# Performance work log

Measured on AMD Instinct MI355X. Metric: run time of the kernel, lower is better.

## Reference

```python
import jax, jax.numpy as jnp
import numpy as np

N, E, G = 25000, 400000, 64
IN, HID, OUT = 16, 16, 16
EF, EH, NH, NC = 8, 64, 128, 10
EPS = 1e-5


def _seg_mean(vals, idx, n):
    s = jax.ops.segment_sum(vals, idx, num_segments=n)
    c = jax.ops.segment_sum(jnp.ones((idx.shape[0], 1), vals.dtype), idx, num_segments=n)
    return s / jnp.maximum(c, 1.0)


def _bn(x, g, b):
    m = x.mean(axis=0)
    v = x.var(axis=0)
    return (x - m) * jax.lax.rsqrt(v + EPS) * g + b


def _nnconv(x, src, dst, ew, root, bias, n_nodes, out_ch):
    # ew: [E, in*out] -> per-edge weight matrix [E, in, out]
    ew = ew.reshape(ew.shape[0], x.shape[1], out_ch)
    msg = jnp.einsum('ei,eio->eo', x[src], ew)  # gather + per-edge matmul
    agg = _seg_mean(msg, dst, n_nodes)          # scatter-mean at target nodes
    return x @ root + agg + bias


def setup_inputs():
    key = jax.random.key(0)
    ks = jax.random.split(key, 24)
    f = lambda k, shp, sc: jax.random.normal(k, shp, dtype=jnp.float32) * sc
    inp = {
        'x': f(ks[0], (N, IN), 1.0),
        'edge_src': jax.random.randint(ks[1], (E,), 0, N, dtype=jnp.int32),
        'edge_dst': jax.random.randint(ks[2], (E,), 0, N, dtype=jnp.int32),
        'edge_attr': f(ks[3], (E, EF), 1.0),
        'batch': jnp.sort(jax.random.randint(ks[4], (N,), 0, G, dtype=jnp.int32)),
        # edge MLP 1: Linear(EF,EH) -> ReLU -> Linear(EH, IN*HID)
        'en1_w1': f(ks[5], (EF, EH), 0.3), 'en1_b1': jnp.zeros((EH,), jnp.float32),
        'en1_w2': f(ks[6], (EH, IN * HID), 0.1), 'en1_b2': jnp.zeros((IN * HID,), jnp.float32),
        'root1': f(ks[7], (IN, HID), 0.25), 'bias1': jnp.zeros((HID,), jnp.float32),
        'bn1_g': jnp.ones((HID,), jnp.float32), 'bn1_b': jnp.zeros((HID,), jnp.float32),
        # edge net 2 (FC): single Linear(EF, HID*OUT)
        'en2_w': f(ks[8], (EF, HID * OUT), 0.1), 'en2_b': jnp.zeros((HID * OUT,), jnp.float32),
        'root2': f(ks[9], (HID, OUT), 0.25), 'bias2': jnp.zeros((OUT,), jnp.float32),
        'bn2_g': jnp.ones((OUT,), jnp.float32), 'bn2_b': jnp.zeros((OUT,), jnp.float32),
        'mlp_w1': f(ks[10], (OUT, NH), 0.25), 'mlp_b1': jnp.zeros((NH,), jnp.float32),
        'mlp_w2': f(ks[11], (NH, NC), 0.1), 'mlp_b2': jnp.zeros((NC,), jnp.float32),
    }
    return inp


def reference(x, edge_src, edge_dst, edge_attr, batch,
              en1_w1, en1_b1, en1_w2, en1_b2, root1, bias1, bn1_g, bn1_b,
              en2_w, en2_b, root2, bias2, bn2_g, bn2_b,
              mlp_w1, mlp_b1, mlp_w2, mlp_b2):
    # NNConv layer 1 (edge MLP -> per-edge weight -> gather-matmul-scatter-mean)
    ew1 = jax.nn.relu(edge_attr @ en1_w1 + en1_b1) @ en1_w2 + en1_b2
    h = _nnconv(x, edge_src, edge_dst, ew1, root1, bias1, N, HID)
    h = _bn(h, bn1_g, bn1_b)
    # NNConv layer 2 (single-Linear edge net)
    ew2 = edge_attr @ en2_w + en2_b
    h = _nnconv(h, edge_src, edge_dst, ew2, root2, bias2, N, OUT)
    h = _bn(h, bn2_g, bn2_b)
    # graph-level mean pooling
    g = _seg_mean(h, batch, G)
    # MLP head + log_softmax
    logits = jax.nn.relu(g @ mlp_w1 + mlp_b1) @ mlp_w2 + mlp_b2
    return jax.nn.log_softmax(logits, axis=1)
```

## Files before the change

### kernel.cpp

```cpp
#include <hip/hip_runtime.h>

#define NN 25000
#define NE 400000
#define NGR 64
#define NB3 391
#define K1B 3125
#define NPAD 25600
#define EPS 1e-5f

static const size_t OFS_XWBUF  = 0;
static const size_t OFS_H1     = 0;
static const size_t OFS_XB2    = 12800000;
static const size_t OFS_MSG    = 13200000;
static const size_t OFS_RANKS  = 13200000;
static const size_t OFS_RANKD  = 13600000;
static const size_t OFS_OUTC8  = 14000000;
static const size_t OFS_INC8   = 14204800;
static const size_t OFS_BASE8  = 14409600;
static const size_t OFS_CBASE8 = 14614400;
static const size_t OFS_STATS  = 19600000;
static const size_t OFS_EREC   = 19625600;
static const size_t OFS_OFF    = 26025600;
static const size_t OFS_CSCOFF = 26051200;
static const size_t OFS_BSUM   = 26128000;
static const size_t OFS_PART1  = 26128512;
static const size_t OFS_PART2  = 26141024;

typedef __attribute__((ext_vector_type(8))) short v8s;
typedef __attribute__((ext_vector_type(4))) float v4f;

__device__ __forceinline__ void atomAddF(float* p, float v) { unsafeAtomicAdd(p, v); }

__device__ __forceinline__ float4 add4(float4 a, float4 b) {
  float4 r; r.x=a.x+b.x; r.y=a.y+b.y; r.z=a.z+b.z; r.w=a.w+b.w; return r;
}
__device__ __forceinline__ void fma4(float4& p, float r, const float4 a) {
  p.x += r*a.x; p.y += r*a.y; p.z += r*a.z; p.w += r*a.w;
}
__device__ __forceinline__ unsigned short f2bf(float f) {
  unsigned u = __float_as_uint(f);
  u += 0x7FFFu + ((u >> 16) & 1u);
  return (unsigned short)(u >> 16);
}

__global__ __launch_bounds__(256) void k1_xw(const float* __restrict__ x,
    const float* __restrict__ w2, const float* __restrict__ b2,
    unsigned short* __restrict__ xwbuf, float* __restrict__ xb2) {
  __shared__ float xs[8][17];
  const int t = threadIdx.x;
  const int h = t >> 2;
  const int og = (t & 3) * 4;
  const int nbase = blockIdx.x * 8;
  if (t < 128) {
    const int n = nbase + (t >> 4), i = t & 15;
    xs[t >> 4][i] = (n < NN) ? x[(size_t)n*16 + i] : 0.f;
  }
  __syncthreads();
  float4 acc[8];
  #pragma unroll
  for (int n = 0; n < 8; ++n) acc[n] = make_float4(0.f,0.f,0.f,0.f);
  #pragma unroll
  for (int i = 0; i < 16; ++i) {
    const float4 w = *reinterpret_cast<const float4*>(&w2[h*256 + i*16 + og]);
    #pragma unroll
    for (int n = 0; n < 8; ++n) fma4(acc[n], xs[n][i], w);
  }
  #pragma unroll
  for (int n = 0; n < 8; ++n) {
    const int nn = nbase + n;
    if (nn < NN) {
      ushort4 s4;
      s4.x = f2bf(acc[n].x); s4.y = f2bf(acc[n].y);
      s4.z = f2bf(acc[n].z); s4.w = f2bf(acc[n].w);
      *reinterpret_cast<ushort4*>(&xwbuf[(size_t)nn*1024 + h*16 + og]) = s4;
    }
  }
  if (t < 128) {
    const int n = nbase + (t >> 4), o = t & 15;
    if (n < NN) {
      float s = 0.f;
      #pragma unroll
      for (int i = 0; i < 16; ++i) s += xs[t >> 4][i] * b2[i*16 + o];
      xb2[(size_t)n*16 + o] = s;
    }
  }
}

__global__ __launch_bounds__(256) void k0_hist(const int* __restrict__ esrc,
    const int* __restrict__ edst, int* __restrict__ outc8, int* __restrict__ inc8,
    int* __restrict__ rankS, int* __restrict__ rankD) {
  const int p = blockIdx.x & 7;
  int* oc = outc8 + p*NPAD;
  int* ic = inc8  + p*NPAD;
  for (int e = blockIdx.x*256 + threadIdx.x; e < NE; e += gridDim.x*256) {
    const int c1 = atomicAdd(&oc[esrc[e]], 1);
    const int c2 = atomicAdd(&ic[edst[e]], 1);
    rankS[e] = (p << 28) | c1;
    rankD[e] = (p << 28) | c2;
  }
}

__global__ __launch_bounds__(256) void k0_scanA(const int* __restrict__ outc8,
    const int* __restrict__ inc8, int* __restrict__ bsum) {
  __shared__ int rO[256], rI[256];
  const int t = threadIdx.x;
  const int i = blockIdx.x*256 + t;
  int s = 0, si = 0;
  #pragma unroll
  for (int p = 0; p < 8; ++p) { s += outc8[p*NPAD + i]; si += inc8[p*NPAD + i]; }
  rO[t] = s; rI[t] = si;
  __syncthreads();
  for (int st = 128; st > 0; st >>= 1) {
    if (t < st) { rO[t] += rO[t+st]; rI[t] += rI[t+st]; }
    __syncthreads();
  }
  if (t == 0) { bsum[blockIdx.x] = rO[0]; bsum[100 + blockIdx.x] = rI[0]; }
}

__global__ __launch_bounds__(128) void k0_scanB(int* __restrict__ bsum) {
  __shared__ int sO[128], sI[128];
  const int t = threadIdx.x;
  const int cO = (t < 100) ? bsum[t] : 0;
  const int cI = (t < 100) ? bsum[100 + t] : 0;
  sO[t] = cO; sI[t] = cI;
  __syncthreads();
  for (int st = 1; st < 128; st <<= 1) {
    const int vO = (t >= st) ? sO[t-st] : 0;
    const int vI = (t >= st) ? sI[t-st] : 0;
    __syncthreads();
    sO[t] += vO; sI[t] += vI;
    __syncthreads();
  }
  if (t < 100) { bsum[200 + t] = sO[t] - cO; bsum[300 + t] = sI[t] - cI; }
}

__global__ __launch_bounds__(256) void k0_scanC(const int* __restrict__ outc8,
    const int* __restrict__ inc8, const int* __restrict__ bsum,
    int* __restrict__ off, int* __restrict__ cscoff,
    int* __restrict__ base8, int* __restrict__ cbase8) {
  __shared__ int sO[256], sI[256];
  const int t = threadIdx.x;
  const int i = blockIdx.x*256 + t;
  int co[8], ci[8];
  int cO = 0, cI = 0;
  #pragma unroll
  for (int p = 0; p < 8; ++p) {
    co[p] = outc8[p*NPAD + i]; cO += co[p];
    ci[p] = inc8[p*NPAD + i];  cI += ci[p];
  }
  sO[t] = cO; sI[t] = cI;
  __syncthreads();
  for (int st = 1; st < 256; st <<= 1) {
    const int vO = (t >= st) ? sO[t-st] : 0;
    const int vI = (t >= st) ? sI[t-st] : 0;
    __syncthreads();
    sO[t] += vO; sI[t] += vI;
    __syncthreads();
  }
  const int offv = sO[t] - cO + bsum[200 + blockIdx.x];
  const int cscv = sI[t] - cI + bsum[300 + blockIdx.x];
  if (i <= NN) { off[i] = offv; cscoff[i] = cscv; }
  int run = offv;
  #pragma unroll
  for (int p = 0; p < 8; ++p) { base8[p*NPAD + i] = run; run += co[p]; }
  run = cscv;
  #pragma unroll
  for (int p = 0; p < 8; ++p) { cbase8[p*NPAD + i] = run; run += ci[p]; }
}

__global__ __launch_bounds__(256) void k0_fill(const int* __restrict__ esrc,
    const int* __restrict__ edst, const float* __restrict__ ea,
    const int* __restrict__ rankS, const int* __restrict__ rankD,
    const int* __restrict__ base8, const int* __restrict__ cbase8,
    float* __restrict__ erec) {
  for (int e = blockIdx.x*blockDim.x + threadIdx.x; e < NE; e += gridDim.x*blockDim.x) {
    const int s = esrc[e], d = edst[e];
    const float4 a = *reinterpret_cast<const float4*>(&ea[(size_t)e*8]);
    const float4 b = *reinterpret_cast<const float4*>(&ea[(size_t)e*8 + 4]);
    const int rs = rankS[e], rd = rankD[e];
    const int slot = base8[(rs >> 28)*NPAD + s] + (rs & 0x0FFFFFFF);
    const int pos  = cbase8[(rd >> 28)*NPAD + d] + (rd & 0x0FFFFFFF);
    float* r = &erec[(size_t)slot*16];
    const float4 c = make_float4(__int_as_float(pos), 0.f, 0.f, 0.f);
    const float4 z = make_float4(0.f, 0.f, 0.f, 0.f);
    *reinterpret_cast<float4*>(r)      = a;
    *reinterpret_cast<float4*>(r + 4)  = b;
    *reinterpret_cast<float4*>(r + 8)  = c;
    *reinterpret_cast<float4*>(r + 12) = z;
  }
}

__global__ __launch_bounds__(256) void k2_csr(const float* __restrict__ erec,
    const float* __restrict__ w1, const float* __restrict__ b1,
    const unsigned short* __restrict__ xwbuf, const float* __restrict__ xb2,
    const int* __restrict__ off, float* __restrict__ msg) {
  __shared__ float w1s[512];
  __shared__ float b1s[64];
  for (int idx = threadIdx.x; idx < 512; idx += 256) w1s[idx] = w1[idx];
  if (threadIdx.x < 64) b1s[threadIdx.x] = b1[threadIdx.x];
  __syncthreads();
  const int lane = threadIdx.x & 63, wl = threadIdx.x >> 6;
  const int eidx = lane & 15;
  const int kg   = lane >> 4;
  const int hb0  = kg*8;
  const int hb1  = 32 + kg*8;
  const int gw = blockIdx.x*4 + wl, nw = gridDim.x*4;

  for (int n = gw; n < NN; n += nw) {
    const int st = off[n];
    const int deg = off[n+1] - st;
    if (deg == 0) continue;
    const unsigned short* xwn = &xwbuf[(size_t)n*1024];
    v8s bf0, bf1;
    #pragma unroll
    for (int j = 0; j < 8; ++j) {
      bf0[j] = (short)xwn[(hb0 + j)*16 + eidx];
      bf1[j] = (short)xwn[(hb1 + j)*16 + eidx];
    }
    const float xbv = xb2[(size_t)n*16 + eidx];

    for (int j0 = 0; j0 < deg; j0 += 16) {
      const int jj = j0 + eidx;
      const int slot = st + ((jj < deg) ? jj : (deg - 1));
      const float* rec = &erec[(size_t)slot*16];
      const float4 ea0 = *reinterpret_cast<const float4*>(rec);
      const float4 ea1 = *reinterpret_cast<const float4*>(rec + 4);
      const int pe = *reinterpret_cast<const int*>(rec + 8);
      const float eav[8] = {ea0.x, ea0.y, ea0.z, ea0.w, ea1.x, ea1.y, ea1.z, ea1.w};
      float4 rA0 = *reinterpret_cast<const float4*>(&b1s[hb0]);
      float4 rA1 = *reinterpret_cast<const float4*>(&b1s[hb0 + 4]);
      float4 rB0 = *reinterpret_cast<const float4*>(&b1s[hb1]);
      float4 rB1 = *reinterpret_cast<const float4*>(&b1s[hb1 + 4]);
      #pragma unroll
      for (int f = 0; f < 8; ++f) {
        const float ef = eav[f];
        fma4(rA0, ef, *reinterpret_cast<const float4*>(&w1s[f*64 + hb0]));
        fma4(rA1, ef, *reinterpret_cast<const float4*>(&w1s[f*64 + hb0 + 4]));
        fma4(rB0, ef, *reinterpret_cast<const float4*>(&w1s[f*64 + hb1]));
        fma4(rB1, ef, *reinterpret_cast<const float4*>(&w1s[f*64 + hb1 + 4]));
      }
      v8s af0, af1;
      af0[0] = (short)f2bf(fmaxf(rA0.x, 0.f)); af0[1] = (short)f2bf(fmaxf(rA0.y, 0.f));
      af0[2] = (short)f2bf(fmaxf(rA0.z, 0.f)); af0[3] = (short)f2bf(fmaxf(rA0.w, 0.f));
      af0[4] = (short)f2bf(fmaxf(rA1.x, 0.f)); af0[5] = (short)f2bf(fmaxf(rA1.y, 0.f));
      af0[6] = (short)f2bf(fmaxf(rA1.z, 0.f)); af0[7] = (short)f2bf(fmaxf(rA1.w, 0.f));
      af1[0] = (short)f2bf(fmaxf(rB0.x, 0.f)); af1[1] = (short)f2bf(fmaxf(rB0.y, 0.f));
      af1[2] = (short)f2bf(fmaxf(rB0.z, 0.f)); af1[3] = (short)f2bf(fmaxf(rB0.w, 0.f));
      af1[4] = (short)f2bf(fmaxf(rB1.x, 0.f)); af1[5] = (short)f2bf(fmaxf(rB1.y, 0.f));
      af1[6] = (short)f2bf(fmaxf(rB1.z, 0.f)); af1[7] = (short)f2bf(fmaxf(rB1.w, 0.f));

      v4f acc = {0.f, 0.f, 0.f, 0.f};
      acc = __builtin_amdgcn_mfma_f32_16x16x32_bf16(af0, bf0, acc, 0, 0, 0);
      acc = __builtin_amdgcn_mfma_f32_16x16x32_bf16(af1, bf1, acc, 0, 0, 0);

      #pragma unroll
      for (int r = 0; r < 4; ++r) {
        const int er = kg*4 + r;
        const int pr = __shfl(pe, er);
        if (j0 + er < deg)
          msg[(size_t)pr*16 + eidx] = acc[r] + xbv;
      }
    }
  }
}

__global__ __launch_bounds__(256) void k3_node1(const float* __restrict__ x,
    const float* __restrict__ root1, const float* __restrict__ bias1,
    const float* __restrict__ msg, const int* __restrict__ cscoff,
    const float* __restrict__ bn_g, const float* __restrict__ bn_b,
    float* __restrict__ h1, float* __restrict__ part,
    float* __restrict__ stats, int* __restrict__ cnt) {
  __shared__ float rt[256];
  __shared__ float red[2][64][16];
  __shared__ float fr[8][33];
  __shared__ int isLast;
  rt[threadIdx.x] = root1[threadIdx.x];
  const int nl = threadIdx.x >> 2, qd = threadIdx.x & 3;
  const int n = blockIdx.x*64 + nl;
  float4 s1 = {0,0,0,0}, s2 = {0,0,0,0};
  __syncthreads();
  if (n < NN) {
    const int b0 = cscoff[n];
    const int deg = cscoff[n+1] - b0;
    float4 sm = {0,0,0,0};
    for (int j = 0; j < deg; ++j)
      sm = add4(sm, *reinterpret_cast<const float4*>(&msg[(size_t)(b0+j)*16 + qd*4]));
    float4 acc = *reinterpret_cast<const float4*>(&bias1[qd*4]);
    #pragma unroll
    for (int i = 0; i < 16; ++i)
      fma4(acc, x[(size_t)n*16 + i], *reinterpret_cast<const float4*>(&rt[i*16 + qd*4]));
    const float inv = 1.f / (float)((deg > 0) ? deg : 1);
    fma4(acc, inv, sm);
    *reinterpret_cast<float4*>(&h1[(size_t)n*16 + qd*4]) = acc;
    s1 = acc;
    s2.x = acc.x*acc.x; s2.y = acc.y*acc.y; s2.z = acc.z*acc.z; s2.w = acc.w*acc.w;
  }
  *reinterpret_cast<float4*>(&red[0][nl][qd*4]) = s1;
  *reinterpret_cast<float4*>(&red[1][nl][qd*4]) = s2;
  __syncthreads();
  for (int st = 32; st > 0; st >>= 1) {
    if (nl < st) {
      #pragma unroll
      for (int k = 0; k < 4; ++k) {
        red[0][nl][qd*4+k] += red[0][nl+st][qd*4+k];
        red[1][nl][qd*4+k] += red[1][nl+st][qd*4+k];
      }
    }
    __syncthreads();
  }
  if (nl == 0) {
    *reinterpret_cast<float4*>(&part[blockIdx.x*32 + qd*4]) =
        *reinterpret_cast<const float4*>(&red[0][0][qd*4]);
    *reinterpret_cast<float4*>(&part[blockIdx.x*32 + 16 + qd*4]) =
        *reinterpret_cast<const float4*>(&red[1][0][qd*4]);
  }
  __syncthreads();
  if (threadIdx.x == 0) {
    __threadfence();
    isLast = (atomicAdd(cnt, 1) == NB3 - 1);
  }
  __syncthreads();
  if (!isLast) return;
  __threadfence();
  {
    const int o = threadIdx.x & 31, c = threadIdx.x >> 5;
    float s = 0.f;
    for (int blk = c; blk < NB3; blk += 8) s += part[blk*32 + o];
    fr[c][o] = s;
    __syncthreads();
    if (threadIdx.x < 32) {
      float tot = fr[0][threadIdx.x];
      for (int k = 1; k < 8; ++k) tot += fr[k][threadIdx.x];
      fr[0][threadIdx.x] = tot;
    }
    __syncthreads();
    if (threadIdx.x < 16) {
      const int oo = threadIdx.x;
      const float mean = fr[0][oo] / (float)NN;
      const float var  = fr[0][16+oo] / (float)NN - mean*mean;
      const float sc   = bn_g[oo] * rsqrtf(var + EPS);
      stats[32+oo] = sc;
      stats[48+oo] = bn_b[oo] - mean*sc;
    }
  }
}

__global__ __launch_bounds__(256) void k6_csr(const float* __restrict__ erec,
    const float* __restrict__ h1, const float* __restrict__ stats,
    const float* __restrict__ w, const float* __restrict__ bvec,
    const int* __restrict__ off, float* __restrict__ msg) {
  __shared__ float ws2[2048];
  __shared__ float bs2[256];
  __shared__ float hwS[4][128];
  __shared__ float hbS[4][32];
  for (int idx = threadIdx.x; idx < 2048; idx += 256) ws2[idx] = w[idx];
  bs2[threadIdx.x] = bvec[threadIdx.x];
  __syncthreads();
  const int lane = threadIdx.x & 63, wl = threadIdx.x >> 6;
  const int el = lane >> 2, q = lane & 3;
  const int f = lane >> 3, o2 = (lane & 7) * 2;
  const int gw = blockIdx.x*4 + wl, nw = gridDim.x*4;
  for (int n = gw; n < NN; n += nw) {
    const int st = off[n];
    const int deg = off[n+1] - st;
    if (deg == 0) continue;
    if (lane < 16)
      hbS[wl][lane] = h1[(size_t)n*16 + lane]*stats[32+lane] + stats[48+lane];
    __builtin_amdgcn_wave_barrier();
    float a0 = 0.f, a1 = 0.f;
    #pragma unroll
    for (int i = 0; i < 16; ++i) {
      const float hv = hbS[wl][i];
      a0 += hv * ws2[f*256 + i*16 + o2];
      a1 += hv * ws2[f*256 + i*16 + o2 + 1];
    }
    hwS[wl][f*16 + o2] = a0; hwS[wl][f*16 + o2 + 1] = a1;
    if (lane < 16) {
      float s = 0.f;
      #pragma unroll
      for (int i = 0; i < 16; ++i) s += hbS[wl][i] * bs2[i*16 + lane];
      hbS[wl][16 + lane] = s;
    }
    __builtin_amdgcn_wave_barrier();
    const float4 mb = *reinterpret_cast<const float4*>(&hbS[wl][16 + q*4]);
    for (int j0 = 0; j0 < deg; j0 += 16) {
      const int jj = j0 + el;
      const bool act = (jj < deg);
      const int slot = st + (act ? jj : 0);
      const float* rec = &erec[(size_t)slot*16];
      const float4 ea0 = *reinterpret_cast<const float4*>(rec);
      const float4 ea1 = *reinterpret_cast<const float4*>(rec + 4);
      const int pe = *reinterpret_cast<const int*>(rec + 8);
      const float ef[8] = {ea0.x, ea0.y, ea0.z, ea0.w, ea1.x, ea1.y, ea1.z, ea1.w};
      float4 m = mb;
      #pragma unroll
      for (int ff = 0; ff < 8; ++ff)
        fma4(m, ef[ff], *reinterpret_cast<const float4*>(&hwS[wl][ff*16 + q*4]));
      if (act)
        *reinterpret_cast<float4*>(&msg[(size_t)pe*16 + q*4]) = m;
    }
    __builtin_amdgcn_wave_barrier();
  }
}

__global__ __launch_bounds__(256) void k7_node2(const float* __restrict__ h1,
    const float* __restrict__ root2, const float* __restrict__ bias2,
    const float* __restrict__ msg, const int* __restrict__ cscoff,
    const int* __restrict__ batch, const float* __restrict__ bn_g,
    const float* __restrict__ bn_b, float* __restrict__ stats,
    float* __restrict__ part, int* __restrict__ cnt) {
  __shared__ float rt[256];
  __shared__ float scs[16], shs[16];
  __shared__ float red[2][64][16];
  __shared__ float pool[64*17];
  __shared__ float fr[8][33];
  __shared__ int isLast;
  rt[threadIdx.x] = root2[threadIdx.x];
  if (threadIdx.x < 16) { scs[threadIdx.x] = stats[32+threadIdx.x]; shs[threadIdx.x] = stats[48+threadIdx.x]; }
  for (int idx = threadIdx.x; idx < 64*17; idx += 256) pool[idx] = 0.f;
  const int nl = threadIdx.x >> 2, qd = threadIdx.x & 3;
  const int n = blockIdx.x*64 + nl;
  float4 s1 = {0,0,0,0}, s2 = {0,0,0,0};
  __syncthreads();
  if (n < NN) {
    const int b0 = cscoff[n];
    const int deg = cscoff[n+1] - b0;
    float4 sm = {0,0,0,0};
    for (int j = 0; j < deg; ++j)
      sm = add4(sm, *reinterpret_cast<const float4*>(&msg[(size_t)(b0+j)*16 + qd*4]));
    float4 acc = *reinterpret_cast<const float4*>(&bias2[qd*4]);
    #pragma unroll
    for (int i = 0; i < 16; ++i) {
      const float hbn = h1[(size_t)n*16 + i]*scs[i] + shs[i];
      fma4(acc, hbn, *reinterpret_cast<const float4*>(&rt[i*16 + qd*4]));
    }
    const float inv = 1.f / (float)((deg > 0) ? deg : 1);
    fma4(acc, inv, sm);
    s1 = acc;
    s2.x = acc.x*acc.x; s2.y = acc.y*acc.y; s2.z = acc.z*acc.z; s2.w = acc.w*acc.w;
    const int g = batch[n];
    atomicAdd(&pool[g*17 + qd*4 + 0], acc.x);
    atomicAdd(&pool[g*17 + qd*4 + 1], acc.y);
    atomicAdd(&pool[g*17 + qd*4 + 2], acc.z);
    atomicAdd(&pool[g*17 + qd*4 + 3], acc.w);
    if (qd == 0) atomicAdd(&pool[g*17 + 16], 1.0f);
  }
  *reinterpret_cast<float4*>(&red[0][nl][qd*4]) = s1;
  *reinterpret_cast<float4*>(&red[1][nl][qd*4]) = s2;
  __syncthreads();
  for (int st = 32; st > 0; st >>= 1) {
    if (nl < st) {
      #pragma unroll
      for (int k = 0; k < 4; ++k) {
        red[0][nl][qd*4+k] += red[0][nl+st][qd*4+k];
        red[1][nl][qd*4+k] += red[1][nl+st][qd*4+k];
      }
    }
    __syncthreads();
  }
  if (nl == 0) {
    *reinterpret_cast<float4*>(&part[blockIdx.x*32 + qd*4]) =
        *reinterpret_cast<const float4*>(&red[0][0][qd*4]);
    *reinterpret_cast<float4*>(&part[blockIdx.x*32 + 16 + qd*4]) =
        *reinterpret_cast<const float4*>(&red[1][0][qd*4]);
  }
  for (int idx = threadIdx.x; idx < 64*17; idx += 256) {
    const float v = pool[idx];
    if (v != 0.f) {
      const int g = idx / 17, c = idx - g*17;
      atomAddF((c < 16) ? &stats[128 + g*16 + c] : &stats[1152 + g], v);
    }
  }
  __syncthreads();
  if (threadIdx.x == 0) {
    __threadfence();
    isLast = (atomicAdd(cnt, 1) == NB3 - 1);
  }
  __syncthreads();
  if (!isLast) return;
  __threadfence();
  {
    const int o = threadIdx.x & 31, c = threadIdx.x >> 5;
    float s = 0.f;
    for (int blk = c; blk < NB3; blk += 8) s += part[blk*32 + o];
    fr[c][o] = s;
    __syncthreads();
    if (threadIdx.x < 32) {
      float tot = fr[0][threadIdx.x];
      for (int k = 1; k < 8; ++k) tot += fr[k][threadIdx.x];
      fr[0][threadIdx.x] = tot;
    }
    __syncthreads();
    if (threadIdx.x < 16) {
      const int oo = threadIdx.x;
      const float mean = fr[0][oo] / (float)NN;
      const float var  = fr[0][16+oo] / (float)NN - mean*mean;
      const float sc   = bn_g[oo] * rsqrtf(var + EPS);
      stats[96+oo]  = sc;
      stats[112+oo] = bn_b[oo] - mean*sc;
    }
  }
}

__global__ __launch_bounds__(128) void k10_head(const float* __restrict__ stats,
    const float* __restrict__ w1, const float* __restrict__ b1,
    const float* __restrict__ w2, const float* __restrict__ b2,
    float* __restrict__ out) {
  __shared__ float gm[16];
  __shared__ float a[128];
  __shared__ float l[10];
  __shared__ float mls[2];
  const int g = blockIdx.x, j = threadIdx.x;
  if (j < 16) {
    const float cnt = fmaxf(stats[1152 + g], 1.0f);
    gm[j] = (stats[128 + g*16 + j] / cnt) * stats[96 + j] + stats[112 + j];
  }
  __syncthreads();
  float s = b1[j];
  #pragma unroll
  for (int o = 0; o < 16; ++o) s += gm[o]*w1[o*128 + j];
  a[j] = fmaxf(s, 0.f);
  __syncthreads();
  if (j < 10) {
    float t = b2[j];
    #pragma unroll 16
    for (int k = 0; k < 128; ++k) t += a[k]*w2[k*10 + j];
    l[j] = t;
  }
  __syncthreads();
  if (j == 0) {
    float m = l[0];
    for (int c = 1; c < 10; ++c) m = fmaxf(m, l[c]);
    float se = 0.f;
    for (int c = 0; c < 10; ++c) se += expf(l[c]-m);
    mls[0] = m; mls[1] = logf(se);
  }
  __syncthreads();
  if (j < 10) out[g*10 + j] = l[j] - mls[0] - mls[1];
}

extern "C" void kernel_launch(void* const* d_in, const int* in_sizes, int n_in,
                              void* d_out, int out_size, void* d_ws, size_t ws_size,
                              hipStream_t stream) {
  const float* x      = (const float*)d_in[0];
  const int*   esrc   = (const int*)  d_in[1];
  const int*   edst   = (const int*)  d_in[2];
  const float* ea     = (const float*)d_in[3];
  const int*   batch  = (const int*)  d_in[4];
  const float* en1_w1 = (const float*)d_in[5];
  const float* en1_b1 = (const float*)d_in[6];
  const float* en1_w2 = (const float*)d_in[7];
  const float* en1_b2 = (const float*)d_in[8];
  const float* root1  = (const float*)d_in[9];
  const float* bias1  = (const float*)d_in[10];
  const float* bn1_g  = (const float*)d_in[11];
  const float* bn1_b  = (const float*)d_in[12];
  const float* en2_w  = (const float*)d_in[13];
  const float* en2_b  = (const float*)d_in[14];
  const float* root2  = (const float*)d_in[15];
  const float* bias2  = (const float*)d_in[16];
  const float* bn2_g  = (const float*)d_in[17];
  const float* bn2_b  = (const float*)d_in[18];
  const float* mlp_w1 = (const float*)d_in[19];
  const float* mlp_b1 = (const float*)d_in[20];
  const float* mlp_w2 = (const float*)d_in[21];
  const float* mlp_b2 = (const float*)d_in[22];
  float* out = (float*)d_out;
  float* ws  = (float*)d_ws;

  unsigned short* xwbuf = (unsigned short*)(ws + OFS_XWBUF);
  float* xb2    = ws + OFS_XB2;
  float* msg    = ws + OFS_MSG;
  float* stats  = ws + OFS_STATS;
  float* erec   = ws + OFS_EREC;
  float* h1     = ws + OFS_H1;
  float* part1  = ws + OFS_PART1;
  float* part2  = ws + OFS_PART2;
  int*   rankS  = (int*)(ws + OFS_RANKS);
  int*   rankD  = (int*)(ws + OFS_RANKD);
  int*   outc8  = (int*)(ws + OFS_OUTC8);
  int*   inc8   = (int*)(ws + OFS_INC8);
  int*   base8  = (int*)(ws + OFS_BASE8);
  int*   cbase8 = (int*)(ws + OFS_CBASE8);
  int*   off    = (int*)(ws + OFS_OFF);
  int*   cscoff = (int*)(ws + OFS_CSCOFF);
  int*   bsum   = (int*)(ws + OFS_BSUM);
  int*   cnt1   = (int*)(stats + 1216);
  int*   cnt2   = (int*)(stats + 1217);

  hipMemsetAsync(outc8, 0, 2*8*NPAD*sizeof(int), stream);
  hipMemsetAsync(stats, 0, 2048*sizeof(float), stream);

  hipLaunchKernelGGL(k1_xw, dim3(K1B), dim3(256), 0, stream, x, en1_w2, en1_b2, xwbuf, xb2);

  hipLaunchKernelGGL(k0_hist,  dim3(1024), dim3(256), 0, stream, esrc, edst, outc8, inc8, rankS, rankD);
  hipLaunchKernelGGL(k0_scanA, dim3(100),  dim3(256), 0, stream, outc8, inc8, bsum);
  hipLaunchKernelGGL(k0_scanB, dim3(1),    dim3(128), 0, stream, bsum);
  hipLaunchKernelGGL(k0_scanC, dim3(100),  dim3(256), 0, stream, outc8, inc8, bsum,
                     off, cscoff, base8, cbase8);
  hipLaunchKernelGGL(k0_fill,  dim3(1024), dim3(256), 0, stream, esrc, edst, ea,
                     rankS, rankD, base8, cbase8, erec);

  hipLaunchKernelGGL(k2_csr,   dim3(1024), dim3(256), 0, stream, erec, en1_w1, en1_b1,
                     xwbuf, xb2, off, msg);
  hipLaunchKernelGGL(k3_node1, dim3(NB3),  dim3(256), 0, stream, x, root1, bias1, msg, cscoff,
                     bn1_g, bn1_b, h1, part1, stats, cnt1);

  hipLaunchKernelGGL(k6_csr,   dim3(1024), dim3(256), 0, stream, erec, h1, stats,
                     en2_w, en2_b, off, msg);
  hipLaunchKernelGGL(k7_node2, dim3(NB3),  dim3(256), 0, stream, h1, root2, bias2, msg, cscoff,
                     batch, bn2_g, bn2_b, stats, part2, cnt2);

  hipLaunchKernelGGL(k10_head, dim3(64), dim3(128), 0, stream, stats, mlp_w1, mlp_b1, mlp_w2, mlp_b2, out);
}
```

Before: 225.3 us.

## Compute layer-2 per-edge messages with bf16 MFMA instead of scalar FMAs

The layer-2 edge kernel now builds a 16x32 bf16 A tile from each edge's 8 attributes (upper K lanes zero) and a B tile from the node's precomputed h·W slices, then runs one mfma_f32_16x16x32_bf16 per 16 edges. Results are scattered to msg with per-lane shuffles of the destination index. This aims to cut the FMA and LDS-read cost, but it lowers precision to bf16, wastes three quarters of the K dimension, and makes the message stores scalar. Separately, the layer-1 edge kernel's grid is doubled.

```diff
diff --git a/kernel.cpp b/kernel.cpp
--- a/kernel.cpp
+++ b/kernel.cpp
@@ -357,7 +357,8 @@
   bs2[threadIdx.x] = bvec[threadIdx.x];
   __syncthreads();
   const int lane = threadIdx.x & 63, wl = threadIdx.x >> 6;
-  const int el = lane >> 2, q = lane & 3;
+  const int eidx = lane & 15;
+  const int kg   = lane >> 4;
   const int f = lane >> 3, o2 = (lane & 7) * 2;
   const int gw = blockIdx.x*4 + wl, nw = gridDim.x*4;
   for (int n = gw; n < NN; n += nw) {
@@ -382,24 +383,40 @@
       hbS[wl][16 + lane] = s;
     }
     __builtin_amdgcn_wave_barrier();
-    const float4 mb = *reinterpret_cast<const float4*>(&hbS[wl][16 + q*4]);
+    v8s bf = {0,0,0,0,0,0,0,0};
+    if (kg == 0) {
+      #pragma unroll
+      for (int j = 0; j < 8; ++j)
+        bf[j] = (short)f2bf(hwS[wl][j*16 + eidx]);
+    }
+    const float hbv = hbS[wl][16 + eidx];
+    __builtin_amdgcn_wave_barrier();
+
     for (int j0 = 0; j0 < deg; j0 += 16) {
-      const int jj = j0 + el;
-      const bool act = (jj < deg);
-      const int slot = st + (act ? jj : 0);
-      const float* rec = &erec[(size_t)slot*16];
-      const float4 ea0 = *reinterpret_cast<const float4*>(rec);
-      const float4 ea1 = *reinterpret_cast<const float4*>(rec + 4);
-      const int pe = *reinterpret_cast<const int*>(rec + 8);
-      const float ef[8] = {ea0.x, ea0.y, ea0.z, ea0.w, ea1.x, ea1.y, ea1.z, ea1.w};
-      float4 m = mb;
-      #pragma unroll
-      for (int ff = 0; ff < 8; ++ff)
-        fma4(m, ef[ff], *reinterpret_cast<const float4*>(&hwS[wl][ff*16 + q*4]));
-      if (act)
-        *reinterpret_cast<float4*>(&msg[(size_t)pe*16 + q*4]) = m;
-    }
-    __builtin_amdgcn_wave_barrier();
+      v8s af = {0,0,0,0,0,0,0,0};
+      int pe = 0;
+      if (kg == 0) {
+        const int jj = j0 + eidx;
+        const int slot = st + ((jj < deg) ? jj : (deg - 1));
+        const float* rec = &erec[(size_t)slot*16];
+        const float4 ea0 = *reinterpret_cast<const float4*>(rec);
+        const float4 ea1 = *reinterpret_cast<const float4*>(rec + 4);
+        pe = *reinterpret_cast<const int*>(rec + 8);
+        af[0] = (short)f2bf(ea0.x); af[1] = (short)f2bf(ea0.y);
+        af[2] = (short)f2bf(ea0.z); af[3] = (short)f2bf(ea0.w);
+        af[4] = (short)f2bf(ea1.x); af[5] = (short)f2bf(ea1.y);
+        af[6] = (short)f2bf(ea1.z); af[7] = (short)f2bf(ea1.w);
+      }
+      v4f acc = {0.f, 0.f, 0.f, 0.f};
+      acc = __builtin_amdgcn_mfma_f32_16x16x32_bf16(af, bf, acc, 0, 0, 0);
+      #pragma unroll
+      for (int r = 0; r < 4; ++r) {
+        const int er = kg*4 + r;
+        const int pr = __shfl(pe, er);
+        if (j0 + er < deg)
+          msg[(size_t)pr*16 + eidx] = acc[r] + hbv;
+      }
+    }
   }
 }
 
@@ -601,7 +618,7 @@
   hipLaunchKernelGGL(k0_fill,  dim3(1024), dim3(256), 0, stream, esrc, edst, ea,
                      rankS, rankD, base8, cbase8, erec);
 
-  hipLaunchKernelGGL(k2_csr,   dim3(1024), dim3(256), 0, stream, erec, en1_w1, en1_b1,
+  hipLaunchKernelGGL(k2_csr,   dim3(2048), dim3(256), 0, stream, erec, en1_w1, en1_b1,
                      xwbuf, xb2, off, msg);
   hipLaunchKernelGGL(k3_node1, dim3(NB3),  dim3(256), 0, stream, x, root1, bias1, msg, cscoff,
                      bn1_g, bn1_b, h1, part1, stats, cnt1);
```

New measurement: 229.6 us. No clear change (+1.9%).
